# Kernel tuning notes

Measured on AMD Instinct MI355X. Metric: run time of the kernel, lower is better.

## Reference

```python
import jax, jax.numpy as jnp
import numpy as np
from jax import lax

DECAY = 0.1
THRESH = 0.5
LENS = 1.0
D_IN = 2 * 34 * 34  # 2312
HID = 800
NC = 10

@jax.custom_vjp
def act_fun(x):
    return (x > THRESH).astype(x.dtype)

def _act_fwd(x):
    return act_fun(x), x

def _act_bwd(x, g):
    p = jax.nn.sigmoid((x - THRESH) / LENS)
    return (g * p * (1.0 - p) / LENS,)

act_fun.defvjp(_act_fwd, _act_bwd)


def setup_inputs() -> dict:
    key = jax.random.key(0)
    ks = jax.random.split(key, 8)
    B, T = 128, 300
    inp = jax.random.uniform(ks[0], (B, 2, 34, 34, 50), dtype=jnp.float32)
    X = jnp.zeros((B, 2, 34, 34, T), dtype=jnp.float32)
    idx = jax.random.randint(ks[1], (B,), 0, T - 50)
    W1 = jax.random.normal(ks[2], (HID, D_IN), dtype=jnp.float32) * 0.02
    b1 = jnp.zeros((HID,), dtype=jnp.float32)
    W2 = jax.random.normal(ks[3], (NC, HID), dtype=jnp.float32) * 0.03
    b2 = jnp.zeros((NC,), dtype=jnp.float32)
    Wc = jax.random.uniform(ks[4], (1, HID + 4), dtype=jnp.float32)  # ctrl init U(0,1)
    bc = jax.random.uniform(ks[5], (1,), dtype=jnp.float32)
    return {"input": inp, "X": X, "idx": idx, "W1": W1, "b1": b1,
            "W2": W2, "b2": b2, "Wc": Wc, "bc": bc}


def _paste(Xi, clip_i, idx_i):
    # X[i, :, :, :, idx:idx+50] = input[i].view(2,34,34,50)
    return lax.dynamic_update_slice(Xi, clip_i, (0, 0, 0, idx_i))


def reference(input, X, idx, W1, b1, W2, b2, Wc, bc):
    B = X.shape[0]
    T = X.shape[-1]
    X = jax.vmap(_paste)(X, input, idx.astype(jnp.int32))
    xs = jnp.moveaxis(X.reshape(B, D_IN, T), -1, 0)  # [T, B, D_IN]

    t = jnp.arange(T)
    freqs = jnp.stack([
        jnp.ones(T), (t % 2 == 0).astype(jnp.float32),
        (t % 10 == 0).astype(jnp.float32), (t % 100 == 0).astype(jnp.float32),
    ], axis=1).astype(X.dtype)  # [T, 4]
    is_first = (t == 0)

    f32 = X.dtype
    carry0 = (
        jnp.zeros((B, HID), f32), jnp.zeros((B, HID), f32),   # h1_mem, h1_spike
        jnp.zeros((B, NC), f32), jnp.zeros((B, NC), f32),     # h2_mem, h2_spike
        jnp.zeros((B, 1), f32), jnp.zeros((B, 1), f32),       # c_mem, c_spike
        jnp.ones((B, 1), f32), jnp.zeros((B, NC), f32),       # bgt, h2_sumspike
    )

    def step(carry, inps):
        h1m, h1s, h2m, h2s, cm, cs, bgt, sum2 = carry
        x, fq, first = inps
        x_a = jnp.where(first, x, x * cs)
        bgt = jnp.where(cs == 1.0, bgt + 1.0, bgt)
        h1m = h1m * DECAY * (1.0 - h1s) + x_a @ W1.T + b1
        h1s = act_fun(h1m)
        h2m = h2m * DECAY * (1.0 - h2s) + h1s @ W2.T + b2
        h2s = act_fun(h2m)
        c_in = jnp.concatenate(
            [lax.stop_gradient(h1s), jnp.broadcast_to(fq, (B, 4))], axis=1)
        cm = cm * 0.1 * (1.0 - cs) + c_in @ Wc.T + bc
        cs = act_fun(cm)
        sum2 = sum2 + h2s
        return (h1m, h1s, h2m, h2s, cm, cs, bgt, sum2), None

    carry, _ = lax.scan(step, carry0, (xs, freqs, is_first))
    bgt, sum2 = carry[6], carry[7]
    rate = sum2 / bgt
    return rate, X
```

## Files before the change

kernel.cpp:

```cpp
#include <hip/hip_runtime.h>

#define D_IN 2312
#define HID  800
#define NCLS 10
#define BATCH 128
#define TSTEPS 300
#define WIN  50

#define MT 64
#define NT 32
#define BKK 16
#define NTM 100
#define NTN 25
#define GEMM_BLOCKS (NTM * NTN)
#define PASTE_BLOCKS 2048
#define BLK 128
#define TOTQ (BATCH * D_IN * (TSTEPS / 4))

__global__ __launch_bounds__(BLK) void fused_kernel(
    const float* __restrict__ inp,
    const float* __restrict__ W1,
    const int*   __restrict__ idx,
    float*       __restrict__ P,
    float*       __restrict__ outX)
{
  __shared__ float As[BKK][MT];
  __shared__ float Bs[BKK][NT + 4];

  int t  = threadIdx.x;
  int bx = blockIdx.x;

  if (bx < GEMM_BLOCKS) {
    int mt = bx / NTN;
    int nt = bx - mt * NTN;
    int m0 = mt * MT, n0 = nt * NT;

    int am = t & 63;
    int ah = t >> 6;
    int r  = m0 + am;
    int bb = r / 50, ss = r - bb * 50;
    const float* aptr = inp + (size_t)bb * (D_IN * WIN) + ss;

    int bn = t >> 4;
    int bk = t & 15;

    int l  = t & 63;
    int lm = l & 7;
    int ln = l >> 3;
    int tm = ah * 32 + lm * 4;
    int tn = ln * 4;

    float aN[8], bN[4];
#pragma unroll
    for (int q = 0; q < 8; ++q) aN[q] = aptr[(ah * 8 + q) * WIN];
#pragma unroll
    for (int p = 0; p < 4; ++p)
      bN[p] = W1[(size_t)(n0 + bn + 8 * p) * D_IN + bk];

    float acc[4][4] = {};

    for (int k0 = 0; k0 < D_IN; k0 += BKK) {
#pragma unroll
      for (int q = 0; q < 8; ++q) As[ah * 8 + q][am] = aN[q];
#pragma unroll
      for (int p = 0; p < 4; ++p) Bs[bk][bn + 8 * p] = bN[p];
      __syncthreads();

      int kn0 = k0 + BKK;
      if (kn0 + BKK <= D_IN) {
#pragma unroll
        for (int q = 0; q < 8; ++q) aN[q] = aptr[(kn0 + ah * 8 + q) * WIN];
#pragma unroll
        for (int p = 0; p < 4; ++p)
          bN[p] = W1[(size_t)(n0 + bn + 8 * p) * D_IN + kn0 + bk];
      } else if (kn0 < D_IN) {
#pragma unroll
        for (int q = 0; q < 8; ++q) {
          int kk = kn0 + ah * 8 + q;
          aN[q] = (kk < D_IN) ? aptr[kk * WIN] : 0.f;
        }
#pragma unroll
        for (int p = 0; p < 4; ++p) {
          int kk = kn0 + bk;
          bN[p] = (kk < D_IN) ? W1[(size_t)(n0 + bn + 8 * p) * D_IN + kk] : 0.f;
        }
      }

#pragma unroll
      for (int kk = 0; kk < BKK; ++kk) {
        float4 A0 = *(const float4*)&As[kk][tm];
        float4 B0 = *(const float4*)&Bs[kk][tn];
        float av[4] = {A0.x, A0.y, A0.z, A0.w};
        float bv[4] = {B0.x, B0.y, B0.z, B0.w};
#pragma unroll
        for (int i = 0; i < 4; ++i)
#pragma unroll
          for (int j = 0; j < 4; ++j)
            acc[i][j] += av[i] * bv[j];
      }
      __syncthreads();
    }

#pragma unroll
    for (int i = 0; i < 4; ++i) {
      int row = m0 + tm + i;
      *(float4*)&P[(size_t)row * HID + n0 + tn] =
          make_float4(acc[i][0], acc[i][1], acc[i][2], acc[i][3]);
    }
  } else {
    int tid = (bx - GEMM_BLOCKS) * BLK + t;
    const int stride = PASTE_BLOCKS * BLK;
    for (int i = tid; i < TOTQ; i += stride) {
      int q  = i % 75;
      int rd = i / 75;
      int b  = rd / D_IN;
      int d  = rd - b * D_IN;
      int ib = idx[b];
      const float* ip = inp + (size_t)b * (D_IN * WIN) + (size_t)d * WIN;
      int t0 = q * 4;
      float v[4];
#pragma unroll
      for (int e = 0; e < 4; ++e) {
        unsigned w = (unsigned)(t0 + e - ib);
        v[e] = (w < (unsigned)WIN) ? ip[w] : 0.f;
      }
      *(float4*)&outX[(size_t)rd * TSTEPS + t0] = make_float4(v[0], v[1], v[2], v[3]);
    }
  }
}

template <int CTRL>
__device__ __forceinline__ float dpp_add(float s) {
  return s + __int_as_float(__builtin_amdgcn_update_dpp(
      0, __float_as_int(s), CTRL, 0xf, 0xf, true));
}
__device__ __forceinline__ float wave_sum(float s) {
  s = dpp_add<0x111>(s);
  s = dpp_add<0x112>(s);
  s = dpp_add<0x114>(s);
  s = dpp_add<0x118>(s);
  s = dpp_add<0x142>(s);
  s = dpp_add<0x143>(s);
  return __int_as_float(__builtin_amdgcn_readlane(__float_as_int(s), 63));
}

__global__ __launch_bounds__(64, 1) void recur_kernel(
    const float* __restrict__ P,
    const float* __restrict__ W2,
    const float* __restrict__ b2,
    const float* __restrict__ Wc,
    const float* __restrict__ bc,
    const float* __restrict__ b1,
    const int*   __restrict__ idx,
    float*       __restrict__ out)
{
  int L = threadIdx.x;
  int b = blockIdx.x;

  int myidx = idx[b];
  const float* Pb = P + (size_t)b * WIN * HID;

  float m[13], b1r[13], wcr[13];
  float w2r[NCLS][13];
  unsigned smask = 0;
#pragma unroll
  for (int rr = 0; rr < 13; ++rr) {
    int j = L + 64 * rr;
    bool ok = (j < HID);
    m[rr]   = 0.f;
    b1r[rr] = ok ? b1[j] : 0.f;
    wcr[rr] = ok ? Wc[j] : 0.f;
#pragma unroll
    for (int c = 0; c < NCLS; ++c)
      w2r[c][rr] = ok ? W2[c * HID + j] : 0.f;
  }

  float cm = 0.f, cs = 0.f, bgt = 1.f;
  float bc0 = bc[0];
  float wf0 = Wc[HID], wf1 = Wc[HID + 1], wf2 = Wc[HID + 2], wf3 = Wc[HID + 3];

  float h2m[10], h2s[10], sum2[10], b2r[10];
#pragma unroll
  for (int c = 0; c < NCLS; ++c) { h2m[c] = 0.f; h2s[c] = 0.f; sum2[c] = 0.f; b2r[c] = b2[c]; }

  float cur[13];
  {
    unsigned w0 = (unsigned)(0 - myidx);
    if (w0 < (unsigned)WIN) {
      const float* Pr = Pb + (size_t)w0 * HID;
#pragma unroll
      for (int rr = 0; rr < 13; ++rr) {
        int j = L + 64 * rr;
        cur[rr] = (j < HID) ? Pr[j] : 0.f;
      }
    } else {
#pragma unroll
      for (int rr = 0; rr < 13; ++rr) cur[rr] = 0.f;
    }
  }

  for (int step = 0; step < TSTEPS; ++step) {
    float gate = (step == 0) ? 1.f : cs;

    float nxt[13];
    {
      unsigned wn = (unsigned)(step + 1 - myidx);
      if (wn < (unsigned)WIN) {
        const float* Pr = Pb + (size_t)wn * HID;
#pragma unroll
        for (int rr = 0; rr < 13; ++rr) {
          int j = L + 64 * rr;
          nxt[rr] = (j < HID) ? Pr[j] : 0.f;
        }
      } else {
#pragma unroll
        for (int rr = 0; rr < 13; ++rr) nxt[rr] = 0.f;
      }
    }

    unsigned nmask = 0;
#pragma unroll
    for (int rr = 0; rr < 13; ++rr) {
      float mprev = ((smask >> rr) & 1u) ? 0.f : m[rr] * 0.1f;
      float mv = mprev + cur[rr] * gate + b1r[rr];
      m[rr] = mv;
      nmask |= (mv > 0.5f) ? (1u << rr) : 0u;
    }
    smask = nmask;

    unsigned long long ball = __ballot(smask != 0u);

    float ctrl = 0.f;
    float dot[10];
#pragma unroll
    for (int c = 0; c < NCLS; ++c) dot[c] = 0.f;

    if (ball) {
      float cacc = 0.f;
#pragma unroll
      for (int rr = 0; rr < 13; ++rr) {
        float f = (float)((smask >> rr) & 1u);
        cacc = fmaf(f, wcr[rr], cacc);
      }
      ctrl = wave_sum(cacc);

#pragma unroll
      for (int rr = 0; rr < 13; ++rr) {
        float f = (float)((smask >> rr) & 1u);
#pragma unroll
        for (int c = 0; c < NCLS; ++c)
          dot[c] = fmaf(f, w2r[c][rr], dot[c]);
      }
#pragma unroll
      for (int c = 0; c < NCLS; ++c) dot[c] = wave_sum(dot[c]);
    }

    bgt += (cs == 1.f) ? 1.f : 0.f;
    float fq = wf0;
    if ((step & 1) == 0)   fq += wf1;
    if (step % 10 == 0)    fq += wf2;
    if (step % 100 == 0)   fq += wf3;
    float cv = (cs != 0.f ? 0.f : cm * 0.1f) + ctrl + fq + bc0;
    cm = cv;
    cs = (cv > 0.5f) ? 1.f : 0.f;

#pragma unroll
    for (int c = 0; c < NCLS; ++c) {
      float v = (h2s[c] != 0.f ? 0.f : h2m[c] * 0.1f) + dot[c] + b2r[c];
      h2m[c] = v;
      h2s[c] = (v > 0.5f) ? 1.f : 0.f;
      sum2[c] += h2s[c];
    }

#pragma unroll
    for (int rr = 0; rr < 13; ++rr) cur[rr] = nxt[rr];
  }

  if (L == 0) {
#pragma unroll
    for (int c = 0; c < NCLS; ++c) out[b * NCLS + c] = sum2[c] / bgt;
  }
}

extern "C" void kernel_launch(void* const* d_in, const int* in_sizes, int n_in,
                              void* d_out, int out_size, void* d_ws, size_t ws_size,
                              hipStream_t stream) {
  const float* inp = (const float*)d_in[0];
  const int*   idx = (const int*)d_in[2];
  const float* W1  = (const float*)d_in[3];
  const float* b1  = (const float*)d_in[4];
  const float* W2  = (const float*)d_in[5];
  const float* b2  = (const float*)d_in[6];
  const float* Wc  = (const float*)d_in[7];
  const float* bc  = (const float*)d_in[8];

  float* out = (float*)d_out;
  float* P   = (float*)d_ws;

  fused_kernel<<<GEMM_BLOCKS + PASTE_BLOCKS, BLK, 0, stream>>>(
      inp, W1, idx, P, out + BATCH * NCLS);

  recur_kernel<<<BATCH, 64, 0, stream>>>(P, W2, b2, Wc, bc, b1, idx, out);
}
```

Before: 1.061 ms.

## Overlap paste with recurrence kernel and double-buffer GEMM via async LDS loads

The X paste work moves out of the GEMM launch into extra blocks of the recurrence kernel, so the large paste write can run alongside the latency-bound 128-block recurrence instead of competing with the GEMM. The GEMM is rewritten with double-buffered LDS tiles, and A is loaded through global_load_lds direct-to-LDS copies, removing one barrier per slab and the register staging for A. The risk is that the 64-thread paste blocks interfere with the recurrence blocks. The async copies also need correct waits before the LDS reads, and the code relies on the barrier for that.

```diff
diff --git a/kernel.cpp b/kernel.cpp
--- a/kernel.cpp
+++ b/kernel.cpp
@@ -10,122 +10,123 @@
 #define MT 64
 #define NT 32
 #define BKK 16
+#define NSLAB 145
 #define NTM 100
 #define NTN 25
 #define GEMM_BLOCKS (NTM * NTN)
-#define PASTE_BLOCKS 2048
 #define BLK 128
+#define RPASTE 1920
 #define TOTQ (BATCH * D_IN * (TSTEPS / 4))
 
-__global__ __launch_bounds__(BLK) void fused_kernel(
+__device__ __forceinline__ void async_copy4(const float* g, float* l) {
+  __builtin_amdgcn_global_load_lds(
+      (const __attribute__((address_space(1))) unsigned int*)g,
+      (__attribute__((address_space(3))) unsigned int*)l, 4, 0, 0);
+}
+
+__global__ __launch_bounds__(BLK) void gemm_kernel(
     const float* __restrict__ inp,
     const float* __restrict__ W1,
-    const int*   __restrict__ idx,
-    float*       __restrict__ P,
-    float*       __restrict__ outX)
+    float*       __restrict__ P)
 {
-  __shared__ float As[BKK][MT];
-  __shared__ float Bs[BKK][NT + 4];
+  __shared__ float As[2][BKK][MT];
+  __shared__ float Bs[2][BKK][NT + 4];
 
   int t  = threadIdx.x;
   int bx = blockIdx.x;
 
-  if (bx < GEMM_BLOCKS) {
-    int mt = bx / NTN;
-    int nt = bx - mt * NTN;
-    int m0 = mt * MT, n0 = nt * NT;
-
-    int am = t & 63;
-    int ah = t >> 6;
-    int r  = m0 + am;
-    int bb = r / 50, ss = r - bb * 50;
-    const float* aptr = inp + (size_t)bb * (D_IN * WIN) + ss;
-
-    int bn = t >> 4;
-    int bk = t & 15;
-
-    int l  = t & 63;
-    int lm = l & 7;
-    int ln = l >> 3;
-    int tm = ah * 32 + lm * 4;
-    int tn = ln * 4;
-
-    float aN[8], bN[4];
-#pragma unroll
-    for (int q = 0; q < 8; ++q) aN[q] = aptr[(ah * 8 + q) * WIN];
-#pragma unroll
-    for (int p = 0; p < 4; ++p)
-      bN[p] = W1[(size_t)(n0 + bn + 8 * p) * D_IN + bk];
-
-    float acc[4][4] = {};
-
-    for (int k0 = 0; k0 < D_IN; k0 += BKK) {
-#pragma unroll
-      for (int q = 0; q < 8; ++q) As[ah * 8 + q][am] = aN[q];
-#pragma unroll
-      for (int p = 0; p < 4; ++p) Bs[bk][bn + 8 * p] = bN[p];
-      __syncthreads();
-
-      int kn0 = k0 + BKK;
-      if (kn0 + BKK <= D_IN) {
-#pragma unroll
-        for (int q = 0; q < 8; ++q) aN[q] = aptr[(kn0 + ah * 8 + q) * WIN];
+  int mt = bx / NTN;
+  int nt = bx - mt * NTN;
+  int m0 = mt * MT, n0 = nt * NT;
+
+  int am = t & 63;
+  int ah = t >> 6;
+  int r  = m0 + am;
+  int bb = r / 50, ss = r - bb * 50;
+  const float* aptr = inp + (size_t)bb * (D_IN * WIN) + ss;
+
+  int bn = t >> 4;
+  int bk = t & 15;
+
+  int l  = t & 63;
+  int lm = l & 7;
+  int ln = l >> 3;
+  int tm = ah * 32 + lm * 4;
+  int tn = ln * 4;
+
+#pragma unroll
+  for (int q = 0; q < 8; ++q) {
+    int kr = ah * 8 + q;
+    async_copy4(aptr + (size_t)kr * WIN, &As[0][kr][0]);
+  }
+  float bN[4];
+#pragma unroll
+  for (int p = 0; p < 4; ++p)
+    bN[p] = W1[(size_t)(n0 + bn + 8 * p) * D_IN + bk];
+#pragma unroll
+  for (int p = 0; p < 4; ++p) Bs[0][bk][bn + 8 * p] = bN[p];
+  __syncthreads();
+
+  float acc[4][4] = {};
+
+  for (int s = 0; s < NSLAB; ++s) {
+    int cur = s & 1, nxt = cur ^ 1;
+    int k0n = (s + 1) * BKK;
+    bool stage = (k0n < D_IN);
+
+    if (stage) {
+      int rem = D_IN - k0n;
+      if (rem >= BKK) {
+#pragma unroll
+        for (int q = 0; q < 8; ++q) {
+          int kr = ah * 8 + q;
+          async_copy4(aptr + (size_t)(k0n + kr) * WIN, &As[nxt][kr][0]);
+        }
 #pragma unroll
         for (int p = 0; p < 4; ++p)
-          bN[p] = W1[(size_t)(n0 + bn + 8 * p) * D_IN + kn0 + bk];
-      } else if (kn0 < D_IN) {
+          bN[p] = W1[(size_t)(n0 + bn + 8 * p) * D_IN + k0n + bk];
+      } else {
 #pragma unroll
         for (int q = 0; q < 8; ++q) {
-          int kk = kn0 + ah * 8 + q;
-          aN[q] = (kk < D_IN) ? aptr[kk * WIN] : 0.f;
+          int kr = ah * 8 + q;
+          if (kr < rem)
+            async_copy4(aptr + (size_t)(k0n + kr) * WIN, &As[nxt][kr][0]);
+          else
+            As[nxt][kr][am] = 0.f;
         }
 #pragma unroll
         for (int p = 0; p < 4; ++p) {
-          int kk = kn0 + bk;
-          bN[p] = (kk < D_IN) ? W1[(size_t)(n0 + bn + 8 * p) * D_IN + kk] : 0.f;
+          int kg = k0n + bk;
+          bN[p] = (kg < D_IN) ? W1[(size_t)(n0 + bn + 8 * p) * D_IN + kg] : 0.f;
         }
       }
-
-#pragma unroll
-      for (int kk = 0; kk < BKK; ++kk) {
-        float4 A0 = *(const float4*)&As[kk][tm];
-        float4 B0 = *(const float4*)&Bs[kk][tn];
-        float av[4] = {A0.x, A0.y, A0.z, A0.w};
-        float bv[4] = {B0.x, B0.y, B0.z, B0.w};
-#pragma unroll
-        for (int i = 0; i < 4; ++i)
-#pragma unroll
-          for (int j = 0; j < 4; ++j)
-            acc[i][j] += av[i] * bv[j];
-      }
-      __syncthreads();
-    }
-
-#pragma unroll
-    for (int i = 0; i < 4; ++i) {
-      int row = m0 + tm + i;
-      *(float4*)&P[(size_t)row * HID + n0 + tn] =
-          make_float4(acc[i][0], acc[i][1], acc[i][2], acc[i][3]);
-    }
-  } else {
-    int tid = (bx - GEMM_BLOCKS) * BLK + t;
-    const int stride = PASTE_BLOCKS * BLK;
-    for (int i = tid; i < TOTQ; i += stride) {
-      int q  = i % 75;
-      int rd = i / 75;
-      int b  = rd / D_IN;
-      int d  = rd - b * D_IN;
-      int ib = idx[b];
-      const float* ip = inp + (size_t)b * (D_IN * WIN) + (size_t)d * WIN;
-      int t0 = q * 4;
-      float v[4];
-#pragma unroll
-      for (int e = 0; e < 4; ++e) {
-        unsigned w = (unsigned)(t0 + e - ib);
-        v[e] = (w < (unsigned)WIN) ? ip[w] : 0.f;
-      }
-      *(float4*)&outX[(size_t)rd * TSTEPS + t0] = make_float4(v[0], v[1], v[2], v[3]);
-    }
+    }
+
+#pragma unroll
+    for (int kk = 0; kk < BKK; ++kk) {
+      float4 A0 = *(const float4*)&As[cur][kk][tm];
+      float4 B0 = *(const float4*)&Bs[cur][kk][tn];
+      float av[4] = {A0.x, A0.y, A0.z, A0.w};
+      float bv[4] = {B0.x, B0.y, B0.z, B0.w};
+#pragma unroll
+      for (int i = 0; i < 4; ++i)
+#pragma unroll
+        for (int j = 0; j < 4; ++j)
+          acc[i][j] += av[i] * bv[j];
+    }
+
+    if (stage) {
+#pragma unroll
+      for (int p = 0; p < 4; ++p) Bs[nxt][bk][bn + 8 * p] = bN[p];
+    }
+    if (s + 1 < NSLAB) __syncthreads();
+  }
+
+#pragma unroll
+  for (int i = 0; i < 4; ++i) {
+    int row = m0 + tm + i;
+    *(float4*)&P[(size_t)row * HID + n0 + tn] =
+        make_float4(acc[i][0], acc[i][1], acc[i][2], acc[i][3]);
   }
 }
 
@@ -152,10 +153,34 @@
     const float* __restrict__ bc,
     const float* __restrict__ b1,
     const int*   __restrict__ idx,
-    float*       __restrict__ out)
+    float*       __restrict__ out,
+    const float* __restrict__ inp,
+    float*       __restrict__ outX)
 {
   int L = threadIdx.x;
   int b = blockIdx.x;
+
+  if (b >= BATCH) {
+    int tid = (b - BATCH) * 64 + L;
+    const int stride = RPASTE * 64;
+    for (int i = tid; i < TOTQ; i += stride) {
+      int q  = i % 75;
+      int rd = i / 75;
+      int bb = rd / D_IN;
+      int d  = rd - bb * D_IN;
+      int ib = idx[bb];
+      const float* ip = inp + (size_t)bb * (D_IN * WIN) + (size_t)d * WIN;
+      int t0 = q * 4;
+      float v[4];
+#pragma unroll
+      for (int e = 0; e < 4; ++e) {
+        unsigned w = (unsigned)(t0 + e - ib);
+        v[e] = (w < (unsigned)WIN) ? ip[w] : 0.f;
+      }
+      *(float4*)&outX[(size_t)rd * TSTEPS + t0] = make_float4(v[0], v[1], v[2], v[3]);
+    }
+    return;
+  }
 
   int myidx = idx[b];
   const float* Pb = P + (size_t)b * WIN * HID;
@@ -297,8 +322,8 @@
   float* out = (float*)d_out;
   float* P   = (float*)d_ws;
 
-  fused_kernel<<<GEMM_BLOCKS + PASTE_BLOCKS, BLK, 0, stream>>>(
-      inp, W1, idx, P, out + BATCH * NCLS);
-
-  recur_kernel<<<BATCH, 64, 0, stream>>>(P, W2, b2, Wc, bc, b1, idx, out);
-}
+  gemm_kernel<<<GEMM_BLOCKS, BLK, 0, stream>>>(inp, W1, P);
+
+  recur_kernel<<<BATCH + RPASTE, 64, 0, stream>>>(
+      P, W2, b2, Wc, bc, b1, idx, out, inp, out + BATCH * NCLS);
+}
```

Measured after the change: 1.112 ms. 4.8% more time.

## Move X paste work from GEMM launch into recurrence kernel as extra blocks

Applied to the files above, without the earlier changes.

Splits the fused GEMM+paste kernel so the GEMM launches alone, and appends 1920 paste blocks to the recurrence kernel launch. The recurrence uses only 128 single-wave blocks and is latency-bound, so the bandwidth-heavy X materialisation can run on otherwise idle CUs concurrently with it. The risk is memory-bandwidth contention slowing the recurrence's P loads, and the recurrence now has extra parameters and an early-exit branch.

```diff
diff --git a/kernel.cpp b/kernel.cpp
--- a/kernel.cpp
+++ b/kernel.cpp
@@ -13,16 +13,14 @@
 #define NTM 100
 #define NTN 25
 #define GEMM_BLOCKS (NTM * NTN)
-#define PASTE_BLOCKS 2048
 #define BLK 128
+#define RPASTE 1920
 #define TOTQ (BATCH * D_IN * (TSTEPS / 4))
 
-__global__ __launch_bounds__(BLK) void fused_kernel(
+__global__ __launch_bounds__(BLK) void gemm_kernel(
     const float* __restrict__ inp,
     const float* __restrict__ W1,
-    const int*   __restrict__ idx,
-    float*       __restrict__ P,
-    float*       __restrict__ outX)
+    float*       __restrict__ P)
 {
   __shared__ float As[BKK][MT];
   __shared__ float Bs[BKK][NT + 4];
@@ -30,102 +28,81 @@
   int t  = threadIdx.x;
   int bx = blockIdx.x;
 
-  if (bx < GEMM_BLOCKS) {
-    int mt = bx / NTN;
-    int nt = bx - mt * NTN;
-    int m0 = mt * MT, n0 = nt * NT;
-
-    int am = t & 63;
-    int ah = t >> 6;
-    int r  = m0 + am;
-    int bb = r / 50, ss = r - bb * 50;
-    const float* aptr = inp + (size_t)bb * (D_IN * WIN) + ss;
-
-    int bn = t >> 4;
-    int bk = t & 15;
-
-    int l  = t & 63;
-    int lm = l & 7;
-    int ln = l >> 3;
-    int tm = ah * 32 + lm * 4;
-    int tn = ln * 4;
-
-    float aN[8], bN[4];
-#pragma unroll
-    for (int q = 0; q < 8; ++q) aN[q] = aptr[(ah * 8 + q) * WIN];
-#pragma unroll
-    for (int p = 0; p < 4; ++p)
-      bN[p] = W1[(size_t)(n0 + bn + 8 * p) * D_IN + bk];
-
-    float acc[4][4] = {};
-
-    for (int k0 = 0; k0 < D_IN; k0 += BKK) {
-#pragma unroll
-      for (int q = 0; q < 8; ++q) As[ah * 8 + q][am] = aN[q];
-#pragma unroll
-      for (int p = 0; p < 4; ++p) Bs[bk][bn + 8 * p] = bN[p];
-      __syncthreads();
-
-      int kn0 = k0 + BKK;
-      if (kn0 + BKK <= D_IN) {
-#pragma unroll
-        for (int q = 0; q < 8; ++q) aN[q] = aptr[(kn0 + ah * 8 + q) * WIN];
-#pragma unroll
-        for (int p = 0; p < 4; ++p)
-          bN[p] = W1[(size_t)(n0 + bn + 8 * p) * D_IN + kn0 + bk];
-      } else if (kn0 < D_IN) {
-#pragma unroll
-        for (int q = 0; q < 8; ++q) {
-          int kk = kn0 + ah * 8 + q;
-          aN[q] = (kk < D_IN) ? aptr[kk * WIN] : 0.f;
-        }
-#pragma unroll
-        for (int p = 0; p < 4; ++p) {
-          int kk = kn0 + bk;
-          bN[p] = (kk < D_IN) ? W1[(size_t)(n0 + bn + 8 * p) * D_IN + kk] : 0.f;
-        }
-      }
-
-#pragma unroll
-      for (int kk = 0; kk < BKK; ++kk) {
-        float4 A0 = *(const float4*)&As[kk][tm];
-        float4 B0 = *(const float4*)&Bs[kk][tn];
-        float av[4] = {A0.x, A0.y, A0.z, A0.w};
-        float bv[4] = {B0.x, B0.y, B0.z, B0.w};
-#pragma unroll
-        for (int i = 0; i < 4; ++i)
-#pragma unroll
-          for (int j = 0; j < 4; ++j)
-            acc[i][j] += av[i] * bv[j];
-      }
-      __syncthreads();
-    }
-
-#pragma unroll
-    for (int i = 0; i < 4; ++i) {
-      int row = m0 + tm + i;
-      *(float4*)&P[(size_t)row * HID + n0 + tn] =
-          make_float4(acc[i][0], acc[i][1], acc[i][2], acc[i][3]);
-    }
-  } else {
-    int tid = (bx - GEMM_BLOCKS) * BLK + t;
-    const int stride = PASTE_BLOCKS * BLK;
-    for (int i = tid; i < TOTQ; i += stride) {
-      int q  = i % 75;
-      int rd = i / 75;
-      int b  = rd / D_IN;
-      int d  = rd - b * D_IN;
-      int ib = idx[b];
-      const float* ip = inp + (size_t)b * (D_IN * WIN) + (size_t)d * WIN;
-      int t0 = q * 4;
-      float v[4];
-#pragma unroll
-      for (int e = 0; e < 4; ++e) {
-        unsigned w = (unsigned)(t0 + e - ib);
-        v[e] = (w < (unsigned)WIN) ? ip[w] : 0.f;
-      }
-      *(float4*)&outX[(size_t)rd * TSTEPS + t0] = make_float4(v[0], v[1], v[2], v[3]);
-    }
+  int mt = bx / NTN;
+  int nt = bx - mt * NTN;
+  int m0 = mt * MT, n0 = nt * NT;
+
+  int am = t & 63;
+  int ah = t >> 6;
+  int r  = m0 + am;
+  int bb = r / 50, ss = r - bb * 50;
+  const float* aptr = inp + (size_t)bb * (D_IN * WIN) + ss;
+
+  int bn = t >> 4;
+  int bk = t & 15;
+
+  int l  = t & 63;
+  int lm = l & 7;
+  int ln = l >> 3;
+  int tm = ah * 32 + lm * 4;
+  int tn = ln * 4;
+
+  float aN[8], bN[4];
+#pragma unroll
+  for (int q = 0; q < 8; ++q) aN[q] = aptr[(ah * 8 + q) * WIN];
+#pragma unroll
+  for (int p = 0; p < 4; ++p)
+    bN[p] = W1[(size_t)(n0 + bn + 8 * p) * D_IN + bk];
+
+  float acc[4][4] = {};
+
+  for (int k0 = 0; k0 < D_IN; k0 += BKK) {
+#pragma unroll
+    for (int q = 0; q < 8; ++q) As[ah * 8 + q][am] = aN[q];
+#pragma unroll
+    for (int p = 0; p < 4; ++p) Bs[bk][bn + 8 * p] = bN[p];
+    __syncthreads();
+
+    int kn0 = k0 + BKK;
+    if (kn0 + BKK <= D_IN) {
+#pragma unroll
+      for (int q = 0; q < 8; ++q) aN[q] = aptr[(kn0 + ah * 8 + q) * WIN];
+#pragma unroll
+      for (int p = 0; p < 4; ++p)
+        bN[p] = W1[(size_t)(n0 + bn + 8 * p) * D_IN + kn0 + bk];
+    } else if (kn0 < D_IN) {
+#pragma unroll
+      for (int q = 0; q < 8; ++q) {
+        int kk = kn0 + ah * 8 + q;
+        aN[q] = (kk < D_IN) ? aptr[kk * WIN] : 0.f;
+      }
+#pragma unroll
+      for (int p = 0; p < 4; ++p) {
+        int kk = kn0 + bk;
+        bN[p] = (kk < D_IN) ? W1[(size_t)(n0 + bn + 8 * p) * D_IN + kk] : 0.f;
+      }
+    }
+
+#pragma unroll
+    for (int kk = 0; kk < BKK; ++kk) {
+      float4 A0 = *(const float4*)&As[kk][tm];
+      float4 B0 = *(const float4*)&Bs[kk][tn];
+      float av[4] = {A0.x, A0.y, A0.z, A0.w};
+      float bv[4] = {B0.x, B0.y, B0.z, B0.w};
+#pragma unroll
+      for (int i = 0; i < 4; ++i)
+#pragma unroll
+        for (int j = 0; j < 4; ++j)
+          acc[i][j] += av[i] * bv[j];
+    }
+    __syncthreads();
+  }
+
+#pragma unroll
+  for (int i = 0; i < 4; ++i) {
+    int row = m0 + tm + i;
+    *(float4*)&P[(size_t)row * HID + n0 + tn] =
+        make_float4(acc[i][0], acc[i][1], acc[i][2], acc[i][3]);
   }
 }
 
@@ -152,10 +129,34 @@
     const float* __restrict__ bc,
     const float* __restrict__ b1,
     const int*   __restrict__ idx,
-    float*       __restrict__ out)
+    float*       __restrict__ out,
+    const float* __restrict__ inp,
+    float*       __restrict__ outX)
 {
   int L = threadIdx.x;
   int b = blockIdx.x;
+
+  if (b >= BATCH) {
+    int tid = (b - BATCH) * 64 + L;
+    const int stride = RPASTE * 64;
+    for (int i = tid; i < TOTQ; i += stride) {
+      int q  = i % 75;
+      int rd = i / 75;
+      int bb = rd / D_IN;
+      int d  = rd - bb * D_IN;
+      int ib = idx[bb];
+      const float* ip = inp + (size_t)bb * (D_IN * WIN) + (size_t)d * WIN;
+      int t0 = q * 4;
+      float v[4];
+#pragma unroll
+      for (int e = 0; e < 4; ++e) {
+        unsigned w = (unsigned)(t0 + e - ib);
+        v[e] = (w < (unsigned)WIN) ? ip[w] : 0.f;
+      }
+      *(float4*)&outX[(size_t)rd * TSTEPS + t0] = make_float4(v[0], v[1], v[2], v[3]);
+    }
+    return;
+  }
 
   int myidx = idx[b];
   const float* Pb = P + (size_t)b * WIN * HID;
@@ -297,8 +298,8 @@
   float* out = (float*)d_out;
   float* P   = (float*)d_ws;
 
-  fused_kernel<<<GEMM_BLOCKS + PASTE_BLOCKS, BLK, 0, stream>>>(
-      inp, W1, idx, P, out + BATCH * NCLS);
-
-  recur_kernel<<<BATCH, 64, 0, stream>>>(P, W2, b2, Wc, bc, b1, idx, out);
-}
+  gemm_kernel<<<GEMM_BLOCKS, BLK, 0, stream>>>(inp, W1, P);
+
+  recur_kernel<<<BATCH + RPASTE, 64, 0, stream>>>(
+      P, W2, b2, Wc, bc, b1, idx, out, inp, out + BATCH * NCLS);
+}
```

After: 1.032 ms. 1.03x faster.
